# Optimization experiments

Measured on AMD Instinct MI355X. Metric: run time of the kernel, lower is better.

## Reference

```python
import jax, jax.numpy as jnp
import numpy as np

# EfficientMemoryGEMMWithSoftmax forward: the returned value visible to the
# model is simply result = x1 @ x2 (batched GEMM of softmax probs with V).
# The outlier-statistics / sparse / SVD compression path only affects what is
# cached for the (lossy) backward; the forward output math is exact.

B, H, S, D = 2, 16, 2048, 64

def setup_inputs() -> dict:
    key = jax.random.key(0)
    k1, k2 = jax.random.split(key)
    # x1 ~ softmax probabilities: nonnegative, rows normalized over last axis
    logits = jax.random.normal(k1, (B, H, S, S), dtype=jnp.float32)
    x1 = jax.nn.softmax(logits, axis=-1)
    x2 = jax.random.normal(k2, (B, H, S, D), dtype=jnp.float32)
    return {"x1": x1, "x2": x2}

def reference(x1, x2):
    # [B,H,S,S] @ [B,H,S,D] -> [B,H,S,D]
    return jnp.einsum('bhsk,bhkd->bhsd', x1, x2)
```

## Files before the change

### kernel.cpp

```cpp
#include <hip/hip_runtime.h>
#include <hip/hip_bf16.h>


#define S_DIM 2048
#define D_DIM 64
#define BM 128
#define BK 128
#define NT (S_DIM / BK)
#define LDB (BK + 8)

typedef __attribute__((ext_vector_type(8))) short short8;
typedef __attribute__((ext_vector_type(4))) short short4v;
typedef __attribute__((ext_vector_type(4))) float f32x4;

__device__ __forceinline__ short f2bf(float x) {
    return __builtin_bit_cast(short, __float2bfloat16(x));
}

__global__ __launch_bounds__(512, 4)
void pv_gemm_kernel(const float* __restrict__ x1,
                    const float* __restrict__ x2,
                    float* __restrict__ out) {
    __shared__ short lds_b[2][D_DIM][LDB];

    int bid = blockIdx.x;
    int lb  = (bid & 7) * 64 + (bid >> 3);
    int bh   = lb >> 4;
    int mblk = lb & 15;
    int m0   = mblk * BM;

    int tid  = threadIdx.x;
    int lane = tid & 63;
    int w    = tid >> 6;

    int sd  = tid & 63;
    int skb = tid >> 6;
    const float* x2base = x2 + (size_t)bh * S_DIM * D_DIM + sd;

    int arow = m0 + w * 16 + (lane & 15);
    int kgrp = (lane >> 4) * 8;
    const float* abase = x1 + ((size_t)bh * S_DIM + arow) * S_DIM + kgrp;

    f32x4 acc[4];
#pragma unroll
    for (int i = 0; i < 4; ++i) acc[i] = (f32x4){0.f, 0.f, 0.f, 0.f};

    {
        float rs[16];
#pragma unroll
        for (int i = 0; i < 16; ++i)
            rs[i] = x2base[(size_t)(skb * 16 + i) * D_DIM];
#pragma unroll
        for (int j = 0; j < 4; ++j) {
            short4v v;
            v[0] = f2bf(rs[4 * j + 0]);
            v[1] = f2bf(rs[4 * j + 1]);
            v[2] = f2bf(rs[4 * j + 2]);
            v[3] = f2bf(rs[4 * j + 3]);
            *(short4v*)&lds_b[0][sd][skb * 16 + 4 * j] = v;
        }
    }

    f32x4 rA0[8], rA1[8];
#pragma unroll
    for (int kk = 0; kk < 4; ++kk) {
        rA0[2 * kk]     = __builtin_nontemporal_load((const f32x4*)(abase + kk * 32));
        rA0[2 * kk + 1] = __builtin_nontemporal_load((const f32x4*)(abase + kk * 32 + 4));
    }

#define ITER(T, RBUF, RA_CUR, RA_NXT)                                        \
    {                                                                        \
        __syncthreads();                                                     \
        float rn[16];                                                        \
        if ((T) + 1 < NT) {                                                  \
            const float* p = x2base + (size_t)((T) + 1) * BK * D_DIM;        \
            _Pragma("unroll")                                                \
            for (int i = 0; i < 16; ++i)                                     \
                rn[i] = p[(size_t)(skb * 16 + i) * D_DIM];                   \
            const float* an = abase + (size_t)((T) + 1) * BK;                \
            _Pragma("unroll")                                                \
            for (int kk = 0; kk < 4; ++kk) {                                 \
                RA_NXT[2 * kk] = __builtin_nontemporal_load(                 \
                    (const f32x4*)(an + kk * 32));                           \
                RA_NXT[2 * kk + 1] = __builtin_nontemporal_load(             \
                    (const f32x4*)(an + kk * 32 + 4));                       \
            }                                                                \
        }                                                                    \
        _Pragma("unroll")                                                    \
        for (int kk = 0; kk < 4; ++kk) {                                     \
            short8 a;                                                        \
            a[0] = f2bf(RA_CUR[2 * kk][0]);                                  \
            a[1] = f2bf(RA_CUR[2 * kk][1]);                                  \
            a[2] = f2bf(RA_CUR[2 * kk][2]);                                  \
            a[3] = f2bf(RA_CUR[2 * kk][3]);                                  \
            a[4] = f2bf(RA_CUR[2 * kk + 1][0]);                              \
            a[5] = f2bf(RA_CUR[2 * kk + 1][1]);                              \
            a[6] = f2bf(RA_CUR[2 * kk + 1][2]);                              \
            a[7] = f2bf(RA_CUR[2 * kk + 1][3]);                              \
            _Pragma("unroll")                                                \
            for (int ni = 0; ni < 4; ++ni) {                                 \
                const short8* bp = (const short8*)                           \
                    &lds_b[RBUF][ni * 16 + (lane & 15)][kk * 32 + kgrp];     \
                acc[ni] = __builtin_amdgcn_mfma_f32_16x16x32_bf16(           \
                    a, *bp, acc[ni], 0, 0, 0);                               \
            }                                                                \
        }                                                                    \
        if ((T) + 1 < NT) {                                                  \
            _Pragma("unroll")                                                \
            for (int j = 0; j < 4; ++j) {                                    \
                short4v v;                                                   \
                v[0] = f2bf(rn[4 * j + 0]);                                  \
                v[1] = f2bf(rn[4 * j + 1]);                                  \
                v[2] = f2bf(rn[4 * j + 2]);                                  \
                v[3] = f2bf(rn[4 * j + 3]);                                  \
                *(short4v*)&lds_b[(RBUF) ^ 1][sd][skb * 16 + 4 * j] = v;     \
            }                                                                \
        }                                                                    \
    }

    for (int t = 0; t < NT; t += 2) {
        ITER(t,     0, rA0, rA1);
        ITER(t + 1, 1, rA1, rA0);
    }
#undef ITER

    int col0 = lane & 15;
    int r0   = m0 + w * 16 + ((lane >> 4) << 2);
    float* ob = out + ((size_t)bh * S_DIM + r0) * D_DIM + col0;
#pragma unroll
    for (int ni = 0; ni < 4; ++ni) {
#pragma unroll
        for (int r = 0; r < 4; ++r)
            __builtin_nontemporal_store(acc[ni][r],
                                        ob + (size_t)r * D_DIM + ni * 16);
    }
}

extern "C" void kernel_launch(void* const* d_in, const int* in_sizes, int n_in,
                              void* d_out, int out_size, void* d_ws, size_t ws_size,
                              hipStream_t stream) {
    const float* x1 = (const float*)d_in[0];
    const float* x2 = (const float*)d_in[1];
    float* out = (float*)d_out;

    dim3 grid(512);
    dim3 block(512);
    hipLaunchKernelGGL(pv_gemm_kernel, grid, block, 0, stream, x1, x2, out);
}
```

Before: 122.6 us.

## Deepen B-tile pipeline to four LDS buffers and halve barriers

Expands the LDS ring for the converted V tiles from two to four buffers and prefetches V two tiles ahead. This lets a __syncthreads run only every other K step, cutting barrier stalls in the main loop, which is now fully unrolled. It also replaces the nontemporal loads of x1 and the nontemporal output stores with ordinary accesses. The trade-off is double the LDS footprint, which may lower how many blocks fit per CU, and different cache behavior for the large streamed x1 operand.

```diff
diff --git a/kernel.cpp b/kernel.cpp
--- a/kernel.cpp
+++ b/kernel.cpp
@@ -21,7 +21,7 @@
 void pv_gemm_kernel(const float* __restrict__ x1,
                     const float* __restrict__ x2,
                     float* __restrict__ out) {
-    __shared__ short lds_b[2][D_DIM][LDB];
+    __shared__ short lds_b[4][D_DIM][LDB];
 
     int bid = blockIdx.x;
     int lb  = (bid & 7) * 64 + (bid >> 3);
@@ -46,44 +46,57 @@
     for (int i = 0; i < 4; ++i) acc[i] = (f32x4){0.f, 0.f, 0.f, 0.f};
 
     {
-        float rs[16];
+        float rs0[16], rs1[16];
 #pragma unroll
         for (int i = 0; i < 16; ++i)
-            rs[i] = x2base[(size_t)(skb * 16 + i) * D_DIM];
+            rs0[i] = x2base[(size_t)(skb * 16 + i) * D_DIM];
+        const float* p1 = x2base + (size_t)BK * D_DIM;
+#pragma unroll
+        for (int i = 0; i < 16; ++i)
+            rs1[i] = p1[(size_t)(skb * 16 + i) * D_DIM];
 #pragma unroll
         for (int j = 0; j < 4; ++j) {
             short4v v;
-            v[0] = f2bf(rs[4 * j + 0]);
-            v[1] = f2bf(rs[4 * j + 1]);
-            v[2] = f2bf(rs[4 * j + 2]);
-            v[3] = f2bf(rs[4 * j + 3]);
+            v[0] = f2bf(rs0[4 * j + 0]);
+            v[1] = f2bf(rs0[4 * j + 1]);
+            v[2] = f2bf(rs0[4 * j + 2]);
+            v[3] = f2bf(rs0[4 * j + 3]);
             *(short4v*)&lds_b[0][sd][skb * 16 + 4 * j] = v;
+        }
+#pragma unroll
+        for (int j = 0; j < 4; ++j) {
+            short4v v;
+            v[0] = f2bf(rs1[4 * j + 0]);
+            v[1] = f2bf(rs1[4 * j + 1]);
+            v[2] = f2bf(rs1[4 * j + 2]);
+            v[3] = f2bf(rs1[4 * j + 3]);
+            *(short4v*)&lds_b[1][sd][skb * 16 + 4 * j] = v;
         }
     }
 
     f32x4 rA0[8], rA1[8];
 #pragma unroll
     for (int kk = 0; kk < 4; ++kk) {
-        rA0[2 * kk]     = __builtin_nontemporal_load((const f32x4*)(abase + kk * 32));
-        rA0[2 * kk + 1] = __builtin_nontemporal_load((const f32x4*)(abase + kk * 32 + 4));
+        rA0[2 * kk]     = *(const f32x4*)(abase + kk * 32);
+        rA0[2 * kk + 1] = *(const f32x4*)(abase + kk * 32 + 4);
     }
 
-#define ITER(T, RBUF, RA_CUR, RA_NXT)                                        \
+#define STEP(T, BR, BW, RA_CUR, RA_NXT, DOBAR)                               \
     {                                                                        \
-        __syncthreads();                                                     \
+        if (DOBAR) __syncthreads();                                          \
         float rn[16];                                                        \
-        if ((T) + 1 < NT) {                                                  \
-            const float* p = x2base + (size_t)((T) + 1) * BK * D_DIM;        \
+        if ((T) + 2 < NT) {                                                  \
+            const float* p = x2base + (size_t)((T) + 2) * BK * D_DIM;        \
             _Pragma("unroll")                                                \
             for (int i = 0; i < 16; ++i)                                     \
                 rn[i] = p[(size_t)(skb * 16 + i) * D_DIM];                   \
+        }                                                                    \
+        if ((T) + 1 < NT) {                                                  \
             const float* an = abase + (size_t)((T) + 1) * BK;                \
             _Pragma("unroll")                                                \
             for (int kk = 0; kk < 4; ++kk) {                                 \
-                RA_NXT[2 * kk] = __builtin_nontemporal_load(                 \
-                    (const f32x4*)(an + kk * 32));                           \
-                RA_NXT[2 * kk + 1] = __builtin_nontemporal_load(             \
-                    (const f32x4*)(an + kk * 32 + 4));                       \
+                RA_NXT[2 * kk]     = *(const f32x4*)(an + kk * 32);          \
+                RA_NXT[2 * kk + 1] = *(const f32x4*)(an + kk * 32 + 4);      \
             }                                                                \
         }                                                                    \
         _Pragma("unroll")                                                    \
@@ -100,12 +113,12 @@
             _Pragma("unroll")                                                \
             for (int ni = 0; ni < 4; ++ni) {                                 \
                 const short8* bp = (const short8*)                           \
-                    &lds_b[RBUF][ni * 16 + (lane & 15)][kk * 32 + kgrp];     \
+                    &lds_b[BR][ni * 16 + (lane & 15)][kk * 32 + kgrp];       \
                 acc[ni] = __builtin_amdgcn_mfma_f32_16x16x32_bf16(           \
                     a, *bp, acc[ni], 0, 0, 0);                               \
             }                                                                \
         }                                                                    \
-        if ((T) + 1 < NT) {                                                  \
+        if ((T) + 2 < NT) {                                                  \
             _Pragma("unroll")                                                \
             for (int j = 0; j < 4; ++j) {                                    \
                 short4v v;                                                   \
@@ -113,16 +126,28 @@
                 v[1] = f2bf(rn[4 * j + 1]);                                  \
                 v[2] = f2bf(rn[4 * j + 2]);                                  \
                 v[3] = f2bf(rn[4 * j + 3]);                                  \
-                *(short4v*)&lds_b[(RBUF) ^ 1][sd][skb * 16 + 4 * j] = v;     \
+                *(short4v*)&lds_b[BW][sd][skb * 16 + 4 * j] = v;             \
             }                                                                \
         }                                                                    \
     }
 
-    for (int t = 0; t < NT; t += 2) {
-        ITER(t,     0, rA0, rA1);
-        ITER(t + 1, 1, rA1, rA0);
-    }
-#undef ITER
+    STEP(0,  0, 2, rA0, rA1, true)
+    STEP(1,  1, 3, rA1, rA0, false)
+    STEP(2,  2, 0, rA0, rA1, true)
+    STEP(3,  3, 1, rA1, rA0, false)
+    STEP(4,  0, 2, rA0, rA1, true)
+    STEP(5,  1, 3, rA1, rA0, false)
+    STEP(6,  2, 0, rA0, rA1, true)
+    STEP(7,  3, 1, rA1, rA0, false)
+    STEP(8,  0, 2, rA0, rA1, true)
+    STEP(9,  1, 3, rA1, rA0, false)
+    STEP(10, 2, 0, rA0, rA1, true)
+    STEP(11, 3, 1, rA1, rA0, false)
+    STEP(12, 0, 2, rA0, rA1, true)
+    STEP(13, 1, 3, rA1, rA0, false)
+    STEP(14, 2, 0, rA0, rA1, true)
+    STEP(15, 3, 1, rA1, rA0, false)
+#undef STEP
 
     int col0 = lane & 15;
     int r0   = m0 + w * 16 + ((lane >> 4) << 2);
@@ -131,8 +156,7 @@
     for (int ni = 0; ni < 4; ++ni) {
 #pragma unroll
         for (int r = 0; r < 4; ++r)
-            __builtin_nontemporal_store(acc[ni][r],
-                                        ob + (size_t)r * D_DIM + ni * 16);
+            ob[(size_t)r * D_DIM + ni * 16] = acc[ni][r];
     }
 }
 
```

Result: slower. 154.6 us (+26.1%).
